# Performance work log

Measured on AMD Instinct MI355X. Metric: run time of the kernel, lower is better.

Reference implementation:

```python
import jax, jax.numpy as jnp
import numpy as np

W_BIT = 4
OUT_F = 11008
IN_F = 4096
K = 16


def unpack_sign(q_bytes):
    """q_bytes: [n_bytes] int32 holding uint8 values. Little-endian bit order.
    Returns float32 signs in {-1, +1} of shape [OUT_F, IN_F]."""
    bits = (q_bytes[:, None] >> jnp.arange(8, dtype=q_bytes.dtype)) & 1  # [n_bytes, 8]
    signs = (2 * bits - 1).astype(jnp.float32)
    return signs.reshape(OUT_F, IN_F)


def setup_inputs() -> dict:
    key = jax.random.key(0)
    k0, k1, k2, k3 = jax.random.split(key, 4)
    x = jax.random.normal(k0, (4, 2048, IN_F), dtype=jnp.float32)
    # packed sign bits: one byte stores 8 signs; OUT_F*IN_F//8 bytes per bit-plane
    qweight = jax.random.randint(k1, (W_BIT, OUT_F * IN_F // 8), 0, 256, dtype=jnp.int32)
    u = jax.random.normal(k2, (W_BIT, OUT_F, K), dtype=jnp.float32) * 0.05
    vt = jax.random.normal(k3, (W_BIT, K, IN_F), dtype=jnp.float32) * 0.05
    return {"x": x, "qweight": qweight, "u": u, "vt": vt}


def reference(x, qweight, u, vt):
    # Reconstruct full weight: w = sum_i sign_i * (u_i @ vt_i), then GEMM x @ w.T.
    # Loop over the small fixed w_bit count to avoid holding all [OUT,IN] bit-planes at once.
    w = jnp.zeros((OUT_F, IN_F), dtype=x.dtype)
    for i in range(W_BIT):
        signs = unpack_sign(qweight[i])            # [OUT_F, IN_F]
        w = w + signs * (u[i] @ vt[i])             # rank-K reconstruction masked by signs
    return x @ w.T                                  # [B, S, OUT_F]
```

## Files before the change

### kernel.cpp

```cpp
#include <hip/hip_runtime.h>
#include <hip/hip_bf16.h>

#define W_BIT 4
#define OUT_F 11008
#define IN_F 4096
#define KRANK 16
#define M_DIM 8192
#define QW_PLANE (OUT_F * IN_F / 8)

#define N_DIM OUT_F
#define K_DIM 4096
#define NBN 43
#define RW_BLOCKS 5504
#define CV_BLOCKS 1024

typedef __attribute__((ext_vector_type(8))) short short8;
typedef __attribute__((ext_vector_type(4))) float f32x4;

__device__ __forceinline__ short f2bf(float f) {
    union { float f; unsigned u; } v;
    v.f = f;
    unsigned r = v.u + 0x7fffu + ((v.u >> 16) & 1u);
    return (short)(r >> 16);
}

__device__ __forceinline__ void async16(void* lds_p, const void* g) {
    __builtin_amdgcn_global_load_lds(
        (const __attribute__((address_space(1))) unsigned int*)g,
        (__attribute__((address_space(3))) unsigned int*)lds_p,
        16, 0, 0);
}

#define BAR() __builtin_amdgcn_s_barrier()
#define LGKM0() do { asm volatile("s_waitcnt lgkmcnt(0)" ::: "memory"); \
                     __builtin_amdgcn_sched_barrier(0); } while (0)
#define VMC(n) do { asm volatile("s_waitcnt vmcnt(" #n ")" ::: "memory"); \
                    __builtin_amdgcn_sched_barrier(0); } while (0)
#define PRIO1() __builtin_amdgcn_s_setprio(1)
#define PRIO0() __builtin_amdgcn_s_setprio(0)

#define DSR(DST, AV, IMM) \
    asm volatile("ds_read_b128 %0, %1 offset:%2" : "=v"(DST) : "v"(AV), "n"(IMM))

__global__ __launch_bounds__(256) void prep_kernel(
    const float* __restrict__ x, const int* __restrict__ qw,
    const float* __restrict__ u, const float* __restrict__ vt,
    short* __restrict__ xb, short* __restrict__ wb) {
    const int b = blockIdx.x;
    const int t = threadIdx.x;

    if (b >= RW_BLOCKS) {
        const int n8 = (M_DIM * IN_F) / 8;
        int tid = (b - RW_BLOCKS) * 256 + t;
        for (int i = tid; i < n8; i += CV_BLOCKS * 256) {
            f32x4 a = ((const f32x4*)x)[2 * i];
            f32x4 c = ((const f32x4*)x)[2 * i + 1];
            short8 o;
            o[0] = f2bf(a[0]); o[1] = f2bf(a[1]); o[2] = f2bf(a[2]); o[3] = f2bf(a[3]);
            o[4] = f2bf(c[0]); o[5] = f2bf(c[1]); o[6] = f2bf(c[2]); o[7] = f2bf(c[3]);
            ((short8*)xb)[i] = o;
        }
        return;
    }

    __shared__ float vts[64][128];
    __shared__ float us[64][64];

    const int c0 = (b & 31) * 128;
    const int o0 = (b >> 5) * 64;

    {
        const f32x4* vt4 = (const f32x4*)vt;
        const int l32 = t & 31;
        const int r0w = t >> 5;
#pragma unroll
        for (int j = 0; j < 8; ++j) {
            int row = r0w + j * 8;
            ((f32x4*)&vts[row][0])[l32] = vt4[(size_t)row * 1024 + (c0 >> 2) + l32];
        }
    }
    {
        const int o = t & 63, q = t >> 6;
#pragma unroll
        for (int i = 0; i < 4; ++i) {
            f32x4 v = ((const f32x4*)u)[((size_t)i * OUT_F + o0 + o) * 4 + q];
            us[i * 16 + q * 4 + 0][o] = v[0];
            us[i * 16 + q * 4 + 1][o] = v[1];
            us[i * 16 + q * 4 + 2][o] = v[2];
            us[i * 16 + q * 4 + 3][o] = v[3];
        }
    }
    __syncthreads();

    const int to = (t >> 4) * 4;
    const int tc = (t & 15) * 8;

    float wacc[4][8];
#pragma unroll
    for (int r = 0; r < 4; ++r)
#pragma unroll
        for (int c = 0; c < 8; ++c) wacc[r][c] = 0.f;

#pragma unroll
    for (int i = 0; i < W_BIT; ++i) {
        float dot[4][8];
#pragma unroll
        for (int r = 0; r < 4; ++r)
#pragma unroll
            for (int c = 0; c < 8; ++c) dot[r][c] = 0.f;
#pragma unroll
        for (int k = 0; k < KRANK; ++k) {
            f32x4 uv = *(const f32x4*)&us[i * 16 + k][to];
            f32x4 v0 = *(const f32x4*)&vts[i * 16 + k][tc];
            f32x4 v1 = *(const f32x4*)&vts[i * 16 + k][tc + 4];
#pragma unroll
            for (int r = 0; r < 4; ++r) {
#pragma unroll
                for (int c = 0; c < 4; ++c) {
                    dot[r][c]     += uv[r] * v0[c];
                    dot[r][c + 4] += uv[r] * v1[c];
                }
            }
        }
#pragma unroll
        for (int r = 0; r < 4; ++r) {
            unsigned byte = (unsigned)qw[i * QW_PLANE + (((o0 + to + r) * IN_F + c0 + tc) >> 3)];
#pragma unroll
            for (int c = 0; c < 8; ++c)
                wacc[r][c] += ((byte >> c) & 1u) ? dot[r][c] : -dot[r][c];
        }
    }
#pragma unroll
    for (int r = 0; r < 4; ++r) {
        short8 o8;
#pragma unroll
        for (int c = 0; c < 8; ++c) o8[c] = f2bf(wacc[r][c]);
        *(short8*)&wb[(size_t)(o0 + to + r) * IN_F + c0 + tc] = o8;
    }
}

__global__ __launch_bounds__(512, 2) void gemm256_kernel(
    const short* __restrict__ A, const short* __restrict__ B, float* __restrict__ C) {
    extern __shared__ short lds[];

    const int t = threadIdx.x;
    const int lane = t & 63, wid = t >> 6;
    const int wr = wid >> 2, wc = wid & 3;
    const int fr = lane & 15, fq = lane >> 4;

    const int bid = blockIdx.x;
    const int cpx = gridDim.x >> 3;
    const int swzb = (bid & 7) * cpx + (bid >> 3);
    const int bm = swzb / NBN, bn = swzb % NBN;
    const long row0 = (long)bm * 256, col0 = (long)bn * 256;

    const int f7 = fr & 7;
    const int g0 = fq ^ f7;
    const int g1 = (4 + fq) ^ f7;
    const int arow = (wr * 128 + fr) * 64;
    const int brow = (wc * 64 + fr) * 64;
    const unsigned av0 = (unsigned)(size_t)((__attribute__((address_space(3))) short*)lds + arow + g0 * 8);
    const unsigned av1 = (unsigned)(size_t)((__attribute__((address_space(3))) short*)lds + arow + g1 * 8);
    const unsigned bv0 = (unsigned)(size_t)((__attribute__((address_space(3))) short*)lds + 32768 + brow + g0 * 8);
    const unsigned bv1 = (unsigned)(size_t)((__attribute__((address_space(3))) short*)lds + 32768 + brow + g1 * 8);

    const int sswz = (((t & 7) ^ ((t >> 3) & 7)) << 3);
    const short* pA = A + (row0 + (t >> 3)) * (size_t)K_DIM + sswz;
    const short* pB = B + (col0 + (t >> 3)) * (size_t)K_DIM + sswz;

    f32x4 acc[8][4];
#pragma unroll
    for (int m = 0; m < 8; ++m)
#pragma unroll
        for (int n = 0; n < 4; ++n) acc[m][n] = (f32x4)0.f;

    short8 a0[8], a1[8], b0[4], b1[4];

#define STGA(P, H, OFFB) do {                                               \
    async16(&lds[(P) * 16384 + (2 * (H)) * 4096 + t * 8],                   \
            (const char*)(pA + (size_t)(2 * (H)) * 64 * K_DIM) + (OFFB));   \
    async16(&lds[(P) * 16384 + (2 * (H) + 1) * 4096 + t * 8],               \
            (const char*)(pA + (size_t)(2 * (H) + 1) * 64 * K_DIM) + (OFFB)); \
} while (0)
#define STGB(P, H, OFFB) do {                                               \
    async16(&lds[32768 + (P) * 16384 + (2 * (H)) * 4096 + t * 8],           \
            (const char*)(pB + (size_t)(2 * (H)) * 64 * K_DIM) + (OFFB));   \
    async16(&lds[32768 + (P) * 16384 + (2 * (H) + 1) * 4096 + t * 8],       \
            (const char*)(pB + (size_t)(2 * (H) + 1) * 64 * K_DIM) + (OFFB)); \
} while (0)

#define RDA(SET, P, MH) do {                                                \
    DSR(SET[0], av0, ((P) * 16384 + (MH) * 4096 + 0 * 1024) * 2);           \
    DSR(SET[1], av0, ((P) * 16384 + (MH) * 4096 + 1 * 1024) * 2);           \
    DSR(SET[2], av0, ((P) * 16384 + (MH) * 4096 + 2 * 1024) * 2);           \
    DSR(SET[3], av0, ((P) * 16384 + (MH) * 4096 + 3 * 1024) * 2);           \
    DSR(SET[4], av1, ((P) * 16384 + (MH) * 4096 + 0 * 1024) * 2);           \
    DSR(SET[5], av1, ((P) * 16384 + (MH) * 4096 + 1 * 1024) * 2);           \
    DSR(SET[6], av1, ((P) * 16384 + (MH) * 4096 + 2 * 1024) * 2);           \
    DSR(SET[7], av1, ((P) * 16384 + (MH) * 4096 + 3 * 1024) * 2);           \
} while (0)

#define RDB(SET, P, NH) do {                                                \
    DSR(SET[0], bv0, ((P) * 16384 + (NH) * 2048 + 0 * 1024) * 2);           \
    DSR(SET[1], bv0, ((P) * 16384 + (NH) * 2048 + 1 * 1024) * 2);           \
    DSR(SET[2], bv1, ((P) * 16384 + (NH) * 2048 + 0 * 1024) * 2);           \
    DSR(SET[3], bv1, ((P) * 16384 + (NH) * 2048 + 1 * 1024) * 2);           \
} while (0)

#define MMAQ(ASET, BSET, MH, NH) do { PRIO1();                              \
    _Pragma("unroll") for (int m = 0; m < 4; ++m)                           \
        _Pragma("unroll") for (int n = 0; n < 2; ++n) {                     \
            acc[(MH) * 4 + m][(NH) * 2 + n] =                               \
                __builtin_amdgcn_mfma_f32_16x16x32_bf16(                    \
                    ASET[m], BSET[n], acc[(MH) * 4 + m][(NH) * 2 + n], 0, 0, 0); \
            acc[(MH) * 4 + m][(NH) * 2 + n] =                               \
                __builtin_amdgcn_mfma_f32_16x16x32_bf16(                    \
                    ASET[4 + m], BSET[2 + n], acc[(MH) * 4 + m][(NH) * 2 + n], 0, 0, 0); \
        }                                                                   \
    PRIO0(); __builtin_amdgcn_sched_barrier(0); } while (0)

#define TILE(P, OFFB, OFFA) do {                                            \
                                                          \
    RDA(a0, P, 0); RDB(b0, P, 0);                                           \
    STGB(1 - (P), 0, OFFB);                                                 \
    BAR(); LGKM0(); MMAQ(a0, b0, 0, 0); BAR();                              \
                                                          \
    RDA(a1, P, 1);                                                          \
    STGB(1 - (P), 1, OFFB);                                                 \
    BAR(); LGKM0(); MMAQ(a1, b0, 1, 0); BAR();                              \
                                                          \
    RDB(b1, P, 1);                                                          \
    STGA(P, 0, OFFA);                                                       \
    BAR(); LGKM0(); MMAQ(a1, b1, 1, 1); BAR();                              \
                             \
    STGA(P, 1, OFFA);                                                       \
    BAR(); MMAQ(a0, b1, 0, 1); VMC(4); BAR();                               \
} while (0)

    STGA(0, 0, 0); STGA(0, 1, 0);
    STGB(0, 0, 0); STGB(0, 1, 0);
    STGA(1, 0, 128); STGA(1, 1, 128);
    VMC(4);
    BAR();

    for (int it = 0; it < 31; ++it) {
        TILE(0, 128, 256);
        TILE(1, 256, 384);
        pA += 128; pB += 128;
    }

    RDA(a0, 0, 0); RDB(b0, 0, 0);
    STGB(1, 0, 128);
    BAR(); LGKM0(); MMAQ(a0, b0, 0, 0); BAR();
    RDA(a1, 0, 1);
    STGB(1, 1, 128);
    BAR(); LGKM0(); MMAQ(a1, b0, 1, 0); BAR();
    RDB(b1, 0, 1);
    BAR(); LGKM0(); MMAQ(a1, b1, 1, 1); BAR();
    BAR(); MMAQ(a0, b1, 0, 1); VMC(0); BAR();
    RDA(a0, 1, 0); RDB(b0, 1, 0);
    BAR(); LGKM0(); MMAQ(a0, b0, 0, 0); BAR();
    RDA(a1, 1, 1);
    BAR(); LGKM0(); MMAQ(a1, b0, 1, 0); BAR();
    RDB(b1, 1, 1);
    BAR(); LGKM0(); MMAQ(a1, b1, 1, 1); BAR();
    BAR(); MMAQ(a0, b1, 0, 1);

#pragma unroll
    for (int m = 0; m < 8; ++m) {
#pragma unroll
        for (int n = 0; n < 4; ++n) {
            f32x4 v = acc[m][n];
            long r0 = row0 + wr * 128 + m * 16 + fq * 4;
            long cc = col0 + wc * 64 + n * 16 + fr;
#pragma unroll
            for (int jj = 0; jj < 4; ++jj)
                C[(size_t)(r0 + jj) * N_DIM + cc] = v[jj];
        }
    }
#undef STGA
#undef STGB
#undef RDA
#undef RDB
#undef MMAQ
#undef TILE
}

extern "C" void kernel_launch(void* const* d_in, const int* in_sizes, int n_in,
                              void* d_out, int out_size, void* d_ws, size_t ws_size,
                              hipStream_t stream) {
    const float* x  = (const float*)d_in[0];
    const int*   qw = (const int*)d_in[1];
    const float* u  = (const float*)d_in[2];
    const float* vt = (const float*)d_in[3];
    float* out = (float*)d_out;

    const size_t wb_bytes = (size_t)OUT_F * IN_F * 2;
    short* wb = (short*)d_ws;
    short* xb = (short*)((char*)d_ws + wb_bytes);

    (void)hipFuncSetAttribute((const void*)gemm256_kernel,
                              hipFuncAttributeMaxDynamicSharedMemorySize, 131072);

    hipLaunchKernelGGL(prep_kernel, dim3(RW_BLOCKS + CV_BLOCKS), dim3(256), 0, stream,
                       x, qw, u, vt, xb, wb);
    hipLaunchKernelGGL(gemm256_kernel, dim3((M_DIM / 256) * (N_DIM / 256)), dim3(512), 131072,
                       stream, xb, wb, out);
}
```

Baseline: 822.2 us.

## Interleave LDS fragment reads with MFMA issue via inline-asm accumulators

The GEMM main loop is rescheduled so the ds_read_b128 loads for the next quadrant's A/B fragments are issued between MFMA groups, and the next tile's first fragments are prefetched during the last quadrant. Two barriers per quadrant are cut to one. MFMAs move to inline asm with AGPR accumulators, and the vmcnt gate changes from 4 to 2. This aims to hide LDS latency behind matrix work and reduce barrier stalls. The risks are hazards on hand-placed asm operands and register-pressure changes from pinning the accumulators to AGPRs.

Result: faster. 787.2 us (-4.3%).

```diff
diff --git a/kernel.cpp b/kernel.cpp
--- a/kernel.cpp
+++ b/kernel.cpp
@@ -41,6 +41,10 @@
 
 #define DSR(DST, AV, IMM) \
     asm volatile("ds_read_b128 %0, %1 offset:%2" : "=v"(DST) : "v"(AV), "n"(IMM))
+
+#define MFA(D, S0, S1) \
+    asm volatile("v_mfma_f32_16x16x32_bf16 %0, %1, %2, %0" \
+                 : "+a"(D) : "v"(S0), "v"(S1))
 
 __global__ __launch_bounds__(256) void prep_kernel(
     const float* __restrict__ x, const int* __restrict__ qw,
@@ -175,6 +179,9 @@
         for (int n = 0; n < 4; ++n) acc[m][n] = (f32x4)0.f;
 
     short8 a0[8], a1[8], b0[4], b1[4];
+
+#define AOFF(P, MH, M) (((P) * 16384 + (MH) * 4096 + (M) * 1024) * 2)
+#define BOFF(P, NH, N) (((P) * 16384 + (NH) * 2048 + (N) * 1024) * 2)
 
 #define STGA(P, H, OFFB) do {                                               \
     async16(&lds[(P) * 16384 + (2 * (H)) * 4096 + t * 8],                   \
@@ -189,52 +196,63 @@
             (const char*)(pB + (size_t)(2 * (H) + 1) * 64 * K_DIM) + (OFFB)); \
 } while (0)
 
-#define RDA(SET, P, MH) do {                                                \
-    DSR(SET[0], av0, ((P) * 16384 + (MH) * 4096 + 0 * 1024) * 2);           \
-    DSR(SET[1], av0, ((P) * 16384 + (MH) * 4096 + 1 * 1024) * 2);           \
-    DSR(SET[2], av0, ((P) * 16384 + (MH) * 4096 + 2 * 1024) * 2);           \
-    DSR(SET[3], av0, ((P) * 16384 + (MH) * 4096 + 3 * 1024) * 2);           \
-    DSR(SET[4], av1, ((P) * 16384 + (MH) * 4096 + 0 * 1024) * 2);           \
-    DSR(SET[5], av1, ((P) * 16384 + (MH) * 4096 + 1 * 1024) * 2);           \
-    DSR(SET[6], av1, ((P) * 16384 + (MH) * 4096 + 2 * 1024) * 2);           \
-    DSR(SET[7], av1, ((P) * 16384 + (MH) * 4096 + 3 * 1024) * 2);           \
+#define MF4(ASET, BSET, MH, NH, M) do {                                     \
+    MFA(acc[(MH) * 4 + (M)][(NH) * 2 + 0], ASET[M], BSET[0]);               \
+    MFA(acc[(MH) * 4 + (M)][(NH) * 2 + 1], ASET[M], BSET[1]);               \
+    MFA(acc[(MH) * 4 + (M)][(NH) * 2 + 0], ASET[4 + (M)], BSET[2]);         \
+    MFA(acc[(MH) * 4 + (M)][(NH) * 2 + 1], ASET[4 + (M)], BSET[3]);         \
 } while (0)
 
-#define RDB(SET, P, NH) do {                                                \
-    DSR(SET[0], bv0, ((P) * 16384 + (NH) * 2048 + 0 * 1024) * 2);           \
-    DSR(SET[1], bv0, ((P) * 16384 + (NH) * 2048 + 1 * 1024) * 2);           \
-    DSR(SET[2], bv1, ((P) * 16384 + (NH) * 2048 + 0 * 1024) * 2);           \
-    DSR(SET[3], bv1, ((P) * 16384 + (NH) * 2048 + 1 * 1024) * 2);           \
-} while (0)
-
-#define MMAQ(ASET, BSET, MH, NH) do { PRIO1();                              \
-    _Pragma("unroll") for (int m = 0; m < 4; ++m)                           \
-        _Pragma("unroll") for (int n = 0; n < 2; ++n) {                     \
-            acc[(MH) * 4 + m][(NH) * 2 + n] =                               \
-                __builtin_amdgcn_mfma_f32_16x16x32_bf16(                    \
-                    ASET[m], BSET[n], acc[(MH) * 4 + m][(NH) * 2 + n], 0, 0, 0); \
-            acc[(MH) * 4 + m][(NH) * 2 + n] =                               \
-                __builtin_amdgcn_mfma_f32_16x16x32_bf16(                    \
-                    ASET[4 + m], BSET[2 + n], acc[(MH) * 4 + m][(NH) * 2 + n], 0, 0, 0); \
-        }                                                                   \
-    PRIO0(); __builtin_amdgcn_sched_barrier(0); } while (0)
-
-#define TILE(P, OFFB, OFFA) do {                                            \
-                                                          \
-    RDA(a0, P, 0); RDB(b0, P, 0);                                           \
+#define TILE(P, OFFB, OFFA, GATE_N, LAST)  do {                             \
+                    \
+    LGKM0();                                                                \
     STGB(1 - (P), 0, OFFB);                                                 \
-    BAR(); LGKM0(); MMAQ(a0, b0, 0, 0); BAR();                              \
-                                                          \
-    RDA(a1, P, 1);                                                          \
+    PRIO1();                                                                \
+    MF4(a0, b0, 0, 0, 0);                                                   \
+    DSR(a1[0], av0, AOFF(P, 1, 0)); DSR(a1[4], av1, AOFF(P, 1, 0));         \
+    MF4(a0, b0, 0, 0, 1);                                                   \
+    DSR(a1[1], av0, AOFF(P, 1, 1)); DSR(a1[5], av1, AOFF(P, 1, 1));         \
+    MF4(a0, b0, 0, 0, 2);                                                   \
+    DSR(a1[2], av0, AOFF(P, 1, 2)); DSR(a1[6], av1, AOFF(P, 1, 2));         \
+    MF4(a0, b0, 0, 0, 3);                                                   \
+    DSR(a1[3], av0, AOFF(P, 1, 3)); DSR(a1[7], av1, AOFF(P, 1, 3));         \
+    PRIO0(); BAR();                                                         \
+                    \
+    LGKM0();                                                                \
     STGB(1 - (P), 1, OFFB);                                                 \
-    BAR(); LGKM0(); MMAQ(a1, b0, 1, 0); BAR();                              \
-                                                          \
-    RDB(b1, P, 1);                                                          \
+    PRIO1();                                                                \
+    MF4(a1, b0, 1, 0, 0);                                                   \
+    DSR(b1[0], bv0, BOFF(P, 1, 0)); DSR(b1[2], bv1, BOFF(P, 1, 0));         \
+    MF4(a1, b0, 1, 0, 1);                                                   \
+    DSR(b1[1], bv0, BOFF(P, 1, 1)); DSR(b1[3], bv1, BOFF(P, 1, 1));         \
+    MF4(a1, b0, 1, 0, 2);                                                   \
+    MF4(a1, b0, 1, 0, 3);                                                   \
+    PRIO0(); BAR();                                                         \
+      \
+    LGKM0();                                                                \
     STGA(P, 0, OFFA);                                                       \
-    BAR(); LGKM0(); MMAQ(a1, b1, 1, 1); BAR();                              \
-                             \
+    PRIO1();                                                                \
+    MF4(a1, b1, 1, 1, 0); MF4(a1, b1, 1, 1, 1);                             \
+    MF4(a1, b1, 1, 1, 2); MF4(a1, b1, 1, 1, 3);                             \
+    PRIO0(); VMC(GATE_N); BAR();                                            \
+           \
     STGA(P, 1, OFFA);                                                       \
-    BAR(); MMAQ(a0, b1, 0, 1); VMC(4); BAR();                               \
+    PRIO1();                                                                \
+    MF4(a0, b1, 0, 1, 0);                                                   \
+    MF4(a0, b1, 0, 1, 1);                                                   \
+    if (!(LAST)) { DSR(a0[0], av0, AOFF(1 - (P), 0, 0));                    \
+                   DSR(a0[4], av1, AOFF(1 - (P), 0, 0)); }                  \
+    MF4(a0, b1, 0, 1, 2);                                                   \
+    if (!(LAST)) { DSR(a0[1], av0, AOFF(1 - (P), 0, 1));                    \
+                   DSR(a0[5], av1, AOFF(1 - (P), 0, 1)); }                  \
+    MF4(a0, b1, 0, 1, 3);                                                   \
+    if (!(LAST)) {                                                          \
+        DSR(a0[2], av0, AOFF(1 - (P), 0, 2)); DSR(a0[6], av1, AOFF(1 - (P), 0, 2)); \
+        DSR(a0[3], av0, AOFF(1 - (P), 0, 3)); DSR(a0[7], av1, AOFF(1 - (P), 0, 3)); \
+        DSR(b0[0], bv0, BOFF(1 - (P), 0, 0)); DSR(b0[2], bv1, BOFF(1 - (P), 0, 0)); \
+        DSR(b0[1], bv0, BOFF(1 - (P), 0, 1)); DSR(b0[3], bv1, BOFF(1 - (P), 0, 1)); \
+    }                                                                       \
+    PRIO0(); BAR();                                                         \
 } while (0)
 
     STGA(0, 0, 0); STGA(0, 1, 0);
@@ -242,29 +260,80 @@
     STGA(1, 0, 128); STGA(1, 1, 128);
     VMC(4);
     BAR();
+    DSR(a0[0], av0, AOFF(0, 0, 0)); DSR(a0[4], av1, AOFF(0, 0, 0));
+    DSR(a0[1], av0, AOFF(0, 0, 1)); DSR(a0[5], av1, AOFF(0, 0, 1));
+    DSR(a0[2], av0, AOFF(0, 0, 2)); DSR(a0[6], av1, AOFF(0, 0, 2));
+    DSR(a0[3], av0, AOFF(0, 0, 3)); DSR(a0[7], av1, AOFF(0, 0, 3));
+    DSR(b0[0], bv0, BOFF(0, 0, 0)); DSR(b0[2], bv1, BOFF(0, 0, 0));
+    DSR(b0[1], bv0, BOFF(0, 0, 1)); DSR(b0[3], bv1, BOFF(0, 0, 1));
 
     for (int it = 0; it < 31; ++it) {
-        TILE(0, 128, 256);
-        TILE(1, 256, 384);
+        TILE(0, 128, 256, 2, 0);
+        TILE(1, 256, 384, 2, 0);
         pA += 128; pB += 128;
     }
 
-    RDA(a0, 0, 0); RDB(b0, 0, 0);
-    STGB(1, 0, 128);
-    BAR(); LGKM0(); MMAQ(a0, b0, 0, 0); BAR();
-    RDA(a1, 0, 1);
-    STGB(1, 1, 128);
-    BAR(); LGKM0(); MMAQ(a1, b0, 1, 0); BAR();
-    RDB(b1, 0, 1);
-    BAR(); LGKM0(); MMAQ(a1, b1, 1, 1); BAR();
-    BAR(); MMAQ(a0, b1, 0, 1); VMC(0); BAR();
-    RDA(a0, 1, 0); RDB(b0, 1, 0);
-    BAR(); LGKM0(); MMAQ(a0, b0, 0, 0); BAR();
-    RDA(a1, 1, 1);
-    BAR(); LGKM0(); MMAQ(a1, b0, 1, 0); BAR();
-    RDB(b1, 1, 1);
-    BAR(); LGKM0(); MMAQ(a1, b1, 1, 1); BAR();
-    BAR(); MMAQ(a0, b1, 0, 1);
+    LGKM0(); STGB(1, 0, 128);
+    PRIO1();
+    MF4(a0, b0, 0, 0, 0);
+    DSR(a1[0], av0, AOFF(0, 1, 0)); DSR(a1[4], av1, AOFF(0, 1, 0));
+    MF4(a0, b0, 0, 0, 1);
+    DSR(a1[1], av0, AOFF(0, 1, 1)); DSR(a1[5], av1, AOFF(0, 1, 1));
+    MF4(a0, b0, 0, 0, 2);
+    DSR(a1[2], av0, AOFF(0, 1, 2)); DSR(a1[6], av1, AOFF(0, 1, 2));
+    MF4(a0, b0, 0, 0, 3);
+    DSR(a1[3], av0, AOFF(0, 1, 3)); DSR(a1[7], av1, AOFF(0, 1, 3));
+    PRIO0(); BAR();
+    LGKM0(); STGB(1, 1, 128);
+    PRIO1();
+    MF4(a1, b0, 1, 0, 0);
+    DSR(b1[0], bv0, BOFF(0, 1, 0)); DSR(b1[2], bv1, BOFF(0, 1, 0));
+    MF4(a1, b0, 1, 0, 1);
+    DSR(b1[1], bv0, BOFF(0, 1, 1)); DSR(b1[3], bv1, BOFF(0, 1, 1));
+    MF4(a1, b0, 1, 0, 2); MF4(a1, b0, 1, 0, 3);
+    PRIO0(); BAR();
+    LGKM0();
+    PRIO1();
+    MF4(a1, b1, 1, 1, 0); MF4(a1, b1, 1, 1, 1);
+    MF4(a1, b1, 1, 1, 2); MF4(a1, b1, 1, 1, 3);
+    PRIO0(); VMC(0); BAR();
+    PRIO1();
+    MF4(a0, b1, 0, 1, 0); MF4(a0, b1, 0, 1, 1);
+    DSR(a0[0], av0, AOFF(1, 0, 0)); DSR(a0[4], av1, AOFF(1, 0, 0));
+    MF4(a0, b1, 0, 1, 2);
+    DSR(a0[1], av0, AOFF(1, 0, 1)); DSR(a0[5], av1, AOFF(1, 0, 1));
+    MF4(a0, b1, 0, 1, 3);
+    DSR(a0[2], av0, AOFF(1, 0, 2)); DSR(a0[6], av1, AOFF(1, 0, 2));
+    DSR(a0[3], av0, AOFF(1, 0, 3)); DSR(a0[7], av1, AOFF(1, 0, 3));
+    DSR(b0[0], bv0, BOFF(1, 0, 0)); DSR(b0[2], bv1, BOFF(1, 0, 0));
+    DSR(b0[1], bv0, BOFF(1, 0, 1)); DSR(b0[3], bv1, BOFF(1, 0, 1));
+    PRIO0(); BAR();
+    LGKM0();
+    PRIO1();
+    MF4(a0, b0, 0, 0, 0);
+    DSR(a1[0], av0, AOFF(1, 1, 0)); DSR(a1[4], av1, AOFF(1, 1, 0));
+    MF4(a0, b0, 0, 0, 1);
+    DSR(a1[1], av0, AOFF(1, 1, 1)); DSR(a1[5], av1, AOFF(1, 1, 1));
+    MF4(a0, b0, 0, 0, 2);
+    DSR(a1[2], av0, AOFF(1, 1, 2)); DSR(a1[6], av1, AOFF(1, 1, 2));
+    MF4(a0, b0, 0, 0, 3);
+    DSR(a1[3], av0, AOFF(1, 1, 3)); DSR(a1[7], av1, AOFF(1, 1, 3));
+    PRIO0(); BAR();
+    LGKM0();
+    PRIO1();
+    MF4(a1, b0, 1, 0, 0);
+    DSR(b1[0], bv0, BOFF(1, 1, 0)); DSR(b1[2], bv1, BOFF(1, 1, 0));
+    MF4(a1, b0, 1, 0, 1);
+    DSR(b1[1], bv0, BOFF(1, 1, 1)); DSR(b1[3], bv1, BOFF(1, 1, 1));
+    MF4(a1, b0, 1, 0, 2); MF4(a1, b0, 1, 0, 3);
+    PRIO0(); BAR();
+    LGKM0();
+    PRIO1();
+    MF4(a1, b1, 1, 1, 0); MF4(a1, b1, 1, 1, 1);
+    MF4(a1, b1, 1, 1, 2); MF4(a1, b1, 1, 1, 3);
+    MF4(a0, b1, 0, 1, 0); MF4(a0, b1, 0, 1, 1);
+    MF4(a0, b1, 0, 1, 2); MF4(a0, b1, 0, 1, 3);
+    PRIO0();
 
 #pragma unroll
     for (int m = 0; m < 8; ++m) {
@@ -280,10 +349,10 @@
     }
 #undef STGA
 #undef STGB
-#undef RDA
-#undef RDB
-#undef MMAQ
+#undef MF4
 #undef TILE
+#undef AOFF
+#undef BOFF
 }
 
 extern "C" void kernel_launch(void* const* d_in, const int* in_sizes, int n_in,
```

## Interleave LDS reads with MFMAs via inline asm and AGPR accumulators

Applied to the files above, without the earlier changes.

Restructures the GEMM main loop so the ds_read_b128 loads for the next quarter-tile are issued between groups of MFMA instructions instead of in separate read phases. Operands for the next tile are prefetched during the current tile's last MFMA groups, and the epilogue is expressed through the same parameterized TILE macro. MFMAs are emitted as inline asm with accumulators constrained to AGPRs. This aims to hide LDS latency behind matrix math and cut barrier-bound stalls, at the cost of fragile hand-scheduled waits and less compiler freedom.

Result: faster. 772.6 us (-6.0%).

```diff
diff --git a/kernel.cpp b/kernel.cpp
--- a/kernel.cpp
+++ b/kernel.cpp
@@ -41,6 +41,10 @@
 
 #define DSR(DST, AV, IMM) \
     asm volatile("ds_read_b128 %0, %1 offset:%2" : "=v"(DST) : "v"(AV), "n"(IMM))
+
+#define MFA(D, S0, S1) \
+    asm volatile("v_mfma_f32_16x16x32_bf16 %0, %1, %2, %0" \
+                 : "+a"(D) : "v"(S0), "v"(S1))
 
 __global__ __launch_bounds__(256) void prep_kernel(
     const float* __restrict__ x, const int* __restrict__ qw,
@@ -175,6 +179,9 @@
         for (int n = 0; n < 4; ++n) acc[m][n] = (f32x4)0.f;
 
     short8 a0[8], a1[8], b0[4], b1[4];
+
+#define AOFF(P, MH, M) (((P) * 16384 + (MH) * 4096 + (M) * 1024) * 2)
+#define BOFF(P, NH, N) (((P) * 16384 + (NH) * 2048 + (N) * 1024) * 2)
 
 #define STGA(P, H, OFFB) do {                                               \
     async16(&lds[(P) * 16384 + (2 * (H)) * 4096 + t * 8],                   \
@@ -189,52 +196,67 @@
             (const char*)(pB + (size_t)(2 * (H) + 1) * 64 * K_DIM) + (OFFB)); \
 } while (0)
 
-#define RDA(SET, P, MH) do {                                                \
-    DSR(SET[0], av0, ((P) * 16384 + (MH) * 4096 + 0 * 1024) * 2);           \
-    DSR(SET[1], av0, ((P) * 16384 + (MH) * 4096 + 1 * 1024) * 2);           \
-    DSR(SET[2], av0, ((P) * 16384 + (MH) * 4096 + 2 * 1024) * 2);           \
-    DSR(SET[3], av0, ((P) * 16384 + (MH) * 4096 + 3 * 1024) * 2);           \
-    DSR(SET[4], av1, ((P) * 16384 + (MH) * 4096 + 0 * 1024) * 2);           \
-    DSR(SET[5], av1, ((P) * 16384 + (MH) * 4096 + 1 * 1024) * 2);           \
-    DSR(SET[6], av1, ((P) * 16384 + (MH) * 4096 + 2 * 1024) * 2);           \
-    DSR(SET[7], av1, ((P) * 16384 + (MH) * 4096 + 3 * 1024) * 2);           \
+#define MFG(ASET, BSET, MH, NH, KH, MB) do {                                \
+    MFA(acc[(MH) * 4 + (MB) + 0][(NH) * 2 + 0], ASET[(KH) * 4 + (MB) + 0], BSET[(KH) * 2 + 0]); \
+    MFA(acc[(MH) * 4 + (MB) + 0][(NH) * 2 + 1], ASET[(KH) * 4 + (MB) + 0], BSET[(KH) * 2 + 1]); \
+    MFA(acc[(MH) * 4 + (MB) + 1][(NH) * 2 + 0], ASET[(KH) * 4 + (MB) + 1], BSET[(KH) * 2 + 0]); \
+    MFA(acc[(MH) * 4 + (MB) + 1][(NH) * 2 + 1], ASET[(KH) * 4 + (MB) + 1], BSET[(KH) * 2 + 1]); \
 } while (0)
 
-#define RDB(SET, P, NH) do {                                                \
-    DSR(SET[0], bv0, ((P) * 16384 + (NH) * 2048 + 0 * 1024) * 2);           \
-    DSR(SET[1], bv0, ((P) * 16384 + (NH) * 2048 + 1 * 1024) * 2);           \
-    DSR(SET[2], bv1, ((P) * 16384 + (NH) * 2048 + 0 * 1024) * 2);           \
-    DSR(SET[3], bv1, ((P) * 16384 + (NH) * 2048 + 1 * 1024) * 2);           \
-} while (0)
-
-#define MMAQ(ASET, BSET, MH, NH) do { PRIO1();                              \
-    _Pragma("unroll") for (int m = 0; m < 4; ++m)                           \
-        _Pragma("unroll") for (int n = 0; n < 2; ++n) {                     \
-            acc[(MH) * 4 + m][(NH) * 2 + n] =                               \
-                __builtin_amdgcn_mfma_f32_16x16x32_bf16(                    \
-                    ASET[m], BSET[n], acc[(MH) * 4 + m][(NH) * 2 + n], 0, 0, 0); \
-            acc[(MH) * 4 + m][(NH) * 2 + n] =                               \
-                __builtin_amdgcn_mfma_f32_16x16x32_bf16(                    \
-                    ASET[4 + m], BSET[2 + n], acc[(MH) * 4 + m][(NH) * 2 + n], 0, 0, 0); \
-        }                                                                   \
-    PRIO0(); __builtin_amdgcn_sched_barrier(0); } while (0)
-
-#define TILE(P, OFFB, OFFA) do {                                            \
-                                                          \
-    RDA(a0, P, 0); RDB(b0, P, 0);                                           \
-    STGB(1 - (P), 0, OFFB);                                                 \
-    BAR(); LGKM0(); MMAQ(a0, b0, 0, 0); BAR();                              \
-                                                          \
-    RDA(a1, P, 1);                                                          \
-    STGB(1 - (P), 1, OFFB);                                                 \
-    BAR(); LGKM0(); MMAQ(a1, b0, 1, 0); BAR();                              \
-                                                          \
-    RDB(b1, P, 1);                                                          \
-    STGA(P, 0, OFFA);                                                       \
-    BAR(); LGKM0(); MMAQ(a1, b1, 1, 1); BAR();                              \
-                             \
-    STGA(P, 1, OFFA);                                                       \
-    BAR(); MMAQ(a0, b1, 0, 1); VMC(4); BAR();                               \
+#define TILE(P, Q, OFFB, OFFA, SB, SA, HG2, G2V, HG3, G3V, NEXT) do {       \
+                                                              \
+    LGKM0();                                                                \
+    if (SB) STGB(Q, 0, OFFB);                                               \
+    PRIO1();                                                                \
+    MFG(a0, b0, 0, 0, 0, 0);                                                \
+    DSR(b1[0], bv0, BOFF(P, 1, 0)); DSR(b1[1], bv0, BOFF(P, 1, 1));         \
+    MFG(a0, b0, 0, 0, 0, 2);                                                \
+    DSR(b1[2], bv1, BOFF(P, 1, 0)); DSR(b1[3], bv1, BOFF(P, 1, 1));         \
+    MFG(a0, b0, 0, 0, 1, 0);                                                \
+    DSR(a1[0], av0, AOFF(P, 1, 0)); DSR(a1[4], av1, AOFF(P, 1, 0));         \
+    MFG(a0, b0, 0, 0, 1, 2);                                                \
+    PRIO0(); BAR();                                                         \
+                                                              \
+    LGKM0();                                                                \
+    if (SB) STGB(Q, 1, OFFB);                                               \
+    PRIO1();                                                                \
+    MFG(a0, b1, 0, 1, 0, 0);                                                \
+    DSR(a1[1], av0, AOFF(P, 1, 1)); DSR(a1[5], av1, AOFF(P, 1, 1));         \
+    MFG(a0, b1, 0, 1, 0, 2);                                                \
+    DSR(a1[2], av0, AOFF(P, 1, 2)); DSR(a1[6], av1, AOFF(P, 1, 2));         \
+    MFG(a0, b1, 0, 1, 1, 0);                                                \
+    DSR(a1[3], av0, AOFF(P, 1, 3)); DSR(a1[7], av1, AOFF(P, 1, 3));         \
+    MFG(a0, b1, 0, 1, 1, 2);                                                \
+    PRIO0();                                                                \
+    if (HG2) { VMC(G2V); }                                                  \
+    BAR();                                                                  \
+     \
+    LGKM0();                                                                \
+    if (SA) STGA(P, 0, OFFA);                                               \
+    PRIO1();                                                                \
+    MFG(a1, b1, 1, 1, 0, 0);                                                \
+    if (NEXT) { DSR(a0[0], av0, AOFF(Q, 0, 0)); DSR(a0[4], av1, AOFF(Q, 0, 0)); } \
+    MFG(a1, b1, 1, 1, 0, 2);                                                \
+    if (NEXT) { DSR(a0[1], av0, AOFF(Q, 0, 1)); DSR(a0[5], av1, AOFF(Q, 0, 1)); } \
+    MFG(a1, b1, 1, 1, 1, 0);                                                \
+    if (NEXT) { DSR(a0[2], av0, AOFF(Q, 0, 2)); DSR(a0[6], av1, AOFF(Q, 0, 2)); } \
+    MFG(a1, b1, 1, 1, 1, 2);                                                \
+    PRIO0();                                                                \
+    if (HG3) { VMC(G3V); }                                                  \
+    BAR();                                                                  \
+                      \
+    if (SA) STGA(P, 1, OFFA);                                               \
+    PRIO1();                                                                \
+    MFG(a1, b0, 1, 0, 0, 0);                                                \
+    if (NEXT) { DSR(a0[3], av0, AOFF(Q, 0, 3)); DSR(a0[7], av1, AOFF(Q, 0, 3)); } \
+    MFG(a1, b0, 1, 0, 0, 2);                                                \
+    MFG(a1, b0, 1, 0, 1, 0);                                                \
+    MFG(a1, b0, 1, 0, 1, 2);                                                \
+    if (NEXT) {                                                             \
+        DSR(b0[0], bv0, BOFF(Q, 0, 0)); DSR(b0[1], bv0, BOFF(Q, 0, 1));     \
+        DSR(b0[2], bv1, BOFF(Q, 0, 0)); DSR(b0[3], bv1, BOFF(Q, 0, 1));     \
+    }                                                                       \
+    PRIO0(); BAR();                                                         \
 } while (0)
 
     STGA(0, 0, 0); STGA(0, 1, 0);
@@ -242,29 +264,21 @@
     STGA(1, 0, 128); STGA(1, 1, 128);
     VMC(4);
     BAR();
+    DSR(a0[0], av0, AOFF(0, 0, 0)); DSR(a0[4], av1, AOFF(0, 0, 0));
+    DSR(a0[1], av0, AOFF(0, 0, 1)); DSR(a0[5], av1, AOFF(0, 0, 1));
+    DSR(a0[2], av0, AOFF(0, 0, 2)); DSR(a0[6], av1, AOFF(0, 0, 2));
+    DSR(a0[3], av0, AOFF(0, 0, 3)); DSR(a0[7], av1, AOFF(0, 0, 3));
+    DSR(b0[0], bv0, BOFF(0, 0, 0)); DSR(b0[1], bv0, BOFF(0, 0, 1));
+    DSR(b0[2], bv1, BOFF(0, 0, 0)); DSR(b0[3], bv1, BOFF(0, 0, 1));
 
     for (int it = 0; it < 31; ++it) {
-        TILE(0, 128, 256);
-        TILE(1, 256, 384);
+        TILE(0, 1, 128, 256, 1, 1, 1, 4, 1, 2, 1);
+        TILE(1, 0, 256, 384, 1, 1, 1, 4, 1, 2, 1);
         pA += 128; pB += 128;
     }
 
-    RDA(a0, 0, 0); RDB(b0, 0, 0);
-    STGB(1, 0, 128);
-    BAR(); LGKM0(); MMAQ(a0, b0, 0, 0); BAR();
-    RDA(a1, 0, 1);
-    STGB(1, 1, 128);
-    BAR(); LGKM0(); MMAQ(a1, b0, 1, 0); BAR();
-    RDB(b1, 0, 1);
-    BAR(); LGKM0(); MMAQ(a1, b1, 1, 1); BAR();
-    BAR(); MMAQ(a0, b1, 0, 1); VMC(0); BAR();
-    RDA(a0, 1, 0); RDB(b0, 1, 0);
-    BAR(); LGKM0(); MMAQ(a0, b0, 0, 0); BAR();
-    RDA(a1, 1, 1);
-    BAR(); LGKM0(); MMAQ(a1, b0, 1, 0); BAR();
-    RDB(b1, 1, 1);
-    BAR(); LGKM0(); MMAQ(a1, b1, 1, 1); BAR();
-    BAR(); MMAQ(a0, b1, 0, 1);
+    TILE(0, 1, 128, 0, 1, 0, 1, 4, 1, 0, 1);
+    TILE(1, 0, 0, 0, 0, 0, 0, 0, 0, 0, 0);
 
 #pragma unroll
     for (int m = 0; m < 8; ++m) {
@@ -280,10 +294,10 @@
     }
 #undef STGA
 #undef STGB
-#undef RDA
-#undef RDB
-#undef MMAQ
+#undef MFG
 #undef TILE
+#undef AOFF
+#undef BOFF
 }
 
 extern "C" void kernel_launch(void* const* d_in, const int* in_sizes, int n_in,
```
